# Performance work log

Measured on AMD Instinct MI355X. Metric: run time of the kernel, lower is better.

Reference implementation:

```python
import jax, jax.numpy as jnp
import numpy as np

B, C, HD, H, W = 4, 64, 64, 64, 64  # batch, input_dim, hidden_dim, spatial


def conv1x1(x, w, b):
    # x: [B, Cin, H, W], w: [Cout, Cin], b: [Cout]
    return jnp.einsum('oc,bchw->bohw', w, x) + b[None, :, None, None]


def setup_inputs() -> dict:
    key = jax.random.key(0)
    ks = jax.random.split(key, 16)
    sc = lambda cin: 1.0 / np.sqrt(cin)
    d = {
        'h': jax.random.normal(ks[0], (B, C, H, W), jnp.float32),
        'm': jax.random.normal(ks[1], (B, C, H, W), jnp.float32),
        'Wq': jax.random.normal(ks[2], (HD, C), jnp.float32) * sc(C),
        'bq': jnp.zeros((HD,), jnp.float32),
        'Wk': jax.random.normal(ks[3], (HD, C), jnp.float32) * sc(C),
        'bk': jnp.zeros((HD,), jnp.float32),
        'Wk2': jax.random.normal(ks[4], (HD, C), jnp.float32) * sc(C),
        'bk2': jnp.zeros((HD,), jnp.float32),
        'Wv': jax.random.normal(ks[5], (C, C), jnp.float32) * sc(C),
        'bv': jnp.zeros((C,), jnp.float32),
        'Wv2': jax.random.normal(ks[6], (C, C), jnp.float32) * sc(C),
        'bv2': jnp.zeros((C,), jnp.float32),
        'Wz': jax.random.normal(ks[7], (2 * C, 2 * C), jnp.float32) * sc(2 * C),
        'bz': jnp.zeros((2 * C,), jnp.float32),
        'Wm': jax.random.normal(ks[8], (3 * C, 3 * C), jnp.float32) * sc(3 * C),
        'bm': jnp.zeros((3 * C,), jnp.float32),
    }
    return d


def reference(h, m, Wq, bq, Wk, bk, Wk2, bk2, Wv, bv, Wv2, bv2, Wz, bz, Wm, bm):
    b, c, hh, ww = h.shape
    n = hh * ww
    K_h = conv1x1(h, Wk, bk).reshape(b, HD, n)            # [B, HD, N]
    Q_h = conv1x1(h, Wq, bq).reshape(b, HD, n).transpose(0, 2, 1)  # [B, N, HD]
    V_h = conv1x1(h, Wv, bv).reshape(b, c, n)             # [B, C, N]
    K_m = conv1x1(m, Wk2, bk2).reshape(b, HD, n)
    V_m = conv1x1(m, Wv2, bv2).reshape(b, c, n)

    A_h = jax.nn.softmax(jnp.einsum('bnd,bdk->bnk', Q_h, K_h), axis=-1)  # [B, N, N]
    Z_h = jnp.einsum('bnk,bck->bcn', A_h, V_h).reshape(b, c, hh, ww)
    A_m = jax.nn.softmax(jnp.einsum('bnd,bdk->bnk', Q_h, K_m), axis=-1)
    Z_m = jnp.einsum('bnk,bck->bcn', A_m, V_m).reshape(b, c, hh, ww)

    Z = conv1x1(jnp.concatenate([Z_h, Z_m], axis=1), Wz, bz)   # [B, 2C, H, W]
    combined = conv1x1(jnp.concatenate([Z, h], axis=1), Wm, bm)  # [B, 3C, H, W]
    mo, mg, mi = jnp.split(combined, 3, axis=1)
    mi = jax.nn.sigmoid(mi)
    new_m = (1.0 - mi) * m + mi * jnp.tanh(mg)
    new_h = jax.nn.sigmoid(mo) * new_m
    return (new_h, new_m)
```

## Files before the change

### kernel.cpp

```cpp
#include <hip/hip_runtime.h>

#define BN 4
#define NN 4096
#define SPLITK 4
#define KTILE 64
#define LOG2E 1.44269504f
#define MFIX 36.0f

typedef __attribute__((ext_vector_type(8))) __bf16 bf16x8;
typedef __attribute__((ext_vector_type(8))) short s16x8;
typedef __attribute__((ext_vector_type(4))) float f32x4;
typedef unsigned short u16;

__device__ __forceinline__ u16 f2bf(float x) {
  unsigned int u = __builtin_bit_cast(unsigned int, x);
  u = (u + 0x7fffu + ((u >> 16) & 1u)) >> 16;
  return (u16)u;
}
__device__ __forceinline__ u16 f2bfs(float x) {
  __bf16 b = (__bf16)x;
  return __builtin_bit_cast(u16, b);
}
__device__ __forceinline__ float bf2f(u16 s) {
  unsigned int u = ((unsigned int)s) << 16;
  return __builtin_bit_cast(float, u);
}

__device__ __forceinline__ float fexp2(float x) {
#if defined(__HIP_DEVICE_COMPILE__) && __has_builtin(__builtin_amdgcn_exp2f)
  return __builtin_amdgcn_exp2f(x);
#else
  return __builtin_exp2f(x);
#endif
}

__device__ __forceinline__ f32x4 mfma32(bf16x8 a, bf16x8 b, f32x4 c) {
#if defined(__HIP_DEVICE_COMPILE__)
  return __builtin_amdgcn_mfma_f32_16x16x32_bf16(a, b, c, 0, 0, 0);
#else
  (void)a; (void)b;
  return c;
#endif
}

__device__ __forceinline__ void gld16(const u16* g, u16* l) {
#if defined(__HIP_DEVICE_COMPILE__)
  __builtin_amdgcn_global_load_lds(
      (const __attribute__((address_space(1))) void*)g,
      (__attribute__((address_space(3))) void*)l, 16, 0, 0);
#else
  (void)g; (void)l;
#endif
}

#if defined(__HIP_DEVICE_COMPILE__)
#define SETPRIO(p) __builtin_amdgcn_s_setprio(p)
#else
#define SETPRIO(p)
#endif

__global__ __launch_bounds__(256) void fuse_w2_kernel(
    const float* __restrict__ Wz, const float* __restrict__ bz,
    const float* __restrict__ Wm, const float* __restrict__ bm,
    const float* __restrict__ Wq, const float* __restrict__ Wk,
    const float* __restrict__ Wk2, const float* __restrict__ Wv,
    const float* __restrict__ Wv2,
    u16* __restrict__ Wbig, float* __restrict__ bbig, u16* __restrict__ Wall) {
  __shared__ float wrow[128];
  __shared__ float bzs[128];
  int t = threadIdx.x;
  if (blockIdx.x >= 192) {
    int pid = blockIdx.x - 192;
    const float* Wsrc = pid == 0 ? Wq : pid == 1 ? Wk : pid == 2 ? Wk2 : pid == 3 ? Wv : Wv2;
    float sc = (pid == 0) ? LOG2E : 1.f;
#pragma unroll
    for (int i = 0; i < 16; ++i) {
      int idx = t * 16 + i;
      float w = Wsrc[idx] * sc;
      u16 hu = f2bf(w);
      Wall[pid * 4096 + idx] = hu;
      Wall[5 * 4096 + pid * 4096 + idx] = f2bf(w - bf2f(hu));
    }
    return;
  }
  int o = blockIdx.x;
  if (t < 128) { wrow[t] = Wm[o * 192 + t]; bzs[t] = bz[t]; }
  __syncthreads();
  if (t < 128) {
    float s = 0.f;
#pragma unroll 4
    for (int j = 0; j < 128; ++j) s = fmaf(wrow[j], Wz[j * 128 + t], s);
    Wbig[o * 192 + t] = f2bf(s);
  } else if (t < 192) {
    Wbig[o * 192 + t] = f2bf(Wm[o * 192 + t]);
  } else if (t == 192) {
    float s = bm[o];
    for (int j = 0; j < 128; ++j) s = fmaf(wrow[j], bzs[j], s);
    bbig[o] = s;
  }
}

__global__ __launch_bounds__(256) void proj7_kernel(
    const u16* __restrict__ Wall,
    const float* __restrict__ bq, const float* __restrict__ bk,
    const float* __restrict__ bk2, const float* __restrict__ bv,
    const float* __restrict__ bv2,
    const float* __restrict__ h, const float* __restrict__ m,
    u16* __restrict__ Q, u16* __restrict__ Kh, u16* __restrict__ Km,
    u16* __restrict__ Vh, u16* __restrict__ Vm, u16* __restrict__ hT) {
  __shared__ float xs[64][65];
  int blk = blockIdx.x;
  int nt = blk & 63, b = (blk >> 6) & 3, src_m = blk >> 8;
  const float* src = src_m ? m : h;
  int t = threadIdx.x, lane = t & 63, w = t >> 6, col = lane & 15, quad = lane >> 4;
  int n0 = nt * 64;
  {
    int c0 = w * 16, nl = lane;
#pragma unroll
    for (int i = 0; i < 16; ++i)
      xs[c0 + i][nl] = src[((size_t)(b * 64) + c0 + i) * NN + n0 + nl];
  }
  __syncthreads();
  int nloc = w * 16 + col;
  bf16x8 xh[2], xl[2];
#pragma unroll
  for (int half = 0; half < 2; ++half) {
    bf16x8 hh, ll;
#pragma unroll
    for (int j = 0; j < 8; ++j) {
      float x = xs[half * 32 + quad * 8 + j][nloc];
      u16 hu = f2bf(x);
      hh[j] = __builtin_bit_cast(__bf16, hu);
      ll[j] = (__bf16)(x - bf2f(hu));
    }
    xh[half] = hh; xl[half] = ll;
  }
  if (!src_m) {
    int cj = lane & 7, nr = lane >> 3;
#pragma unroll
    for (int it = 0; it < 2; ++it) {
      int n = w * 16 + it * 8 + nr;
      bf16x8 hi8;
#pragma unroll
      for (int i = 0; i < 8; ++i)
        hi8[i] = __builtin_bit_cast(__bf16, f2bf(xs[cj * 8 + i][n]));
      *(bf16x8*)(void*)(hT + ((size_t)b * NN + n0 + n) * 64 + cj * 8) = hi8;
    }
  }
  int glob_n = n0 + nloc;
  auto do_proj = [&](int pid, const float* bias, u16* dstQK, u16* dstV) {
    const u16* Whi = Wall + pid * 4096;
    const u16* Wlo = Wall + 5 * 4096 + pid * 4096;
    float sc = (pid == 0) ? LOG2E : 1.f;
#pragma unroll
    for (int ot = 0; ot < 4; ++ot) {
      size_t wb = (size_t)(ot * 16 + col) * 64 + quad * 8;
      bf16x8 wh0 = *(const bf16x8*)(const void*)(Whi + wb);
      bf16x8 wh1 = *(const bf16x8*)(const void*)(Whi + wb + 32);
      bf16x8 wl0 = *(const bf16x8*)(const void*)(Wlo + wb);
      bf16x8 wl1 = *(const bf16x8*)(const void*)(Wlo + wb + 32);
      float4 b4 = *(const float4*)(bias + ot * 16 + quad * 4);
      f32x4 c = {b4.x * sc, b4.y * sc, b4.z * sc, b4.w * sc};
      c = mfma32(wh0, xh[0], c);
      c = mfma32(wh1, xh[1], c);
      c = mfma32(wh0, xl[0], c);
      c = mfma32(wh1, xl[1], c);
      c = mfma32(wl0, xh[0], c);
      c = mfma32(wl1, xh[1], c);
      if (dstQK) {
        uint2 p;
        p.x = (unsigned)f2bf(c[0]) | ((unsigned)f2bf(c[1]) << 16);
        p.y = (unsigned)f2bf(c[2]) | ((unsigned)f2bf(c[3]) << 16);
        *(uint2*)(void*)(dstQK + ((size_t)b * NN + glob_n) * 64 + ot * 16 + quad * 4) = p;
      } else {
        size_t base = ((size_t)b << 18) + (size_t)(glob_n >> 5) * 2048 + ot * 512 +
                      (size_t)((glob_n >> 3) & 3) * 128 + (glob_n & 7);
#pragma unroll
        for (int r = 0; r < 4; ++r) dstV[base + (quad * 4 + r) * 8] = f2bf(c[r]);
      }
    }
  };
  if (!src_m) {
    do_proj(0, bq, Q, nullptr);
    do_proj(1, bk, Kh, nullptr);
    do_proj(3, bv, nullptr, Vh);
  } else {
    do_proj(2, bk2, Km, nullptr);
    do_proj(4, bv2, nullptr, Vm);
  }
}

__global__ __launch_bounds__(256, 4) void flash14_kernel(
    const u16* __restrict__ Qg, const u16* __restrict__ Khg,
    const u16* __restrict__ Kmg, const u16* __restrict__ Vhg,
    const u16* __restrict__ Vmg, u16* __restrict__ Opart,
    float* __restrict__ Lpart) {
  __shared__ u16 Kl[2][4096];
  __shared__ u16 Vl[3][4096];
  int blk = blockIdx.x;
  int combo = blk & 31, qt = blk >> 5;
  int attn = combo & 1, b = (combo >> 1) & 3, split = combo >> 3;
  const u16* K = (attn ? Kmg : Khg) + (size_t)b * NN * 64;
  const u16* V = (attn ? Vmg : Vhg) + ((size_t)b << 18);
  int t = threadIdx.x, wave = t >> 6, lane = t & 63, col = lane & 15, quad = lane >> 4;
  int row0 = qt * 128 + wave * 32;

  bf16x8 bq[2][2];
#pragma unroll
  for (int g = 0; g < 2; ++g) {
    const u16* qp = Qg + (size_t)b * NN * 64 + (size_t)(row0 + g * 16 + col) * 64 + quad * 8;
    bq[g][0] = *(const bf16x8*)(const void*)qp;
    bq[g][1] = *(const bf16x8*)(const void*)(qp + 32);
  }

  f32x4 O[2][4];
#pragma unroll
  for (int g = 0; g < 2; ++g)
#pragma unroll
    for (int i = 0; i < 4; ++i) O[g][i] = f32x4{0.f, 0.f, 0.f, 0.f};
  f32x4 Lacc[2];
  Lacc[0] = f32x4{0.f, 0.f, 0.f, 0.f};
  Lacc[1] = f32x4{0.f, 0.f, 0.f, 0.f};
  bf16x8 pa[2][2];
#pragma unroll
  for (int grp = 0; grp < 2; ++grp)
#pragma unroll
    for (int g = 0; g < 2; ++g) pa[grp][g] = bf16x8{};
  const f32x4 minit = {-MFIX, -MFIX, -MFIX, -MFIX};
  s16x8 onesv;
#pragma unroll
  for (int i = 0; i < 8; ++i) onesv[i] = (short)0x3F80;
  bf16x8 ones8 = __builtin_bit_cast(bf16x8, onesv);
  int sp = split * 8 + b * 2 + attn;

  const int kbase = split * (NN / SPLITK);
  const int TILES = NN / SPLITK / KTILE;

#define STAGE(KB, VB, K0)                                                        \
  _Pragma("unroll") for (int jj = 0; jj < 2; ++jj) {                             \
    int p = jj * 256 + t;                                                        \
    int krow_ = p >> 3;                                                          \
    int kj_ = (p & 7) ^ (krow_ & 7);                                             \
    int s5_ = krow_ & 31;                                                        \
    int tr_ = (krow_ & 32) | ((s5_ & 12) << 1) | (((s5_ >> 4) & 1) << 2) | (s5_ & 3); \
    gld16(K + (size_t)((K0) + tr_) * 64 + kj_ * 8, (KB) + p * 8);                \
    gld16(V + (size_t)(K0) * 64 + p * 8, (VB) + p * 8);                          \
  }

  STAGE(&Kl[0][0], &Vl[0][0], kbase);
  int vs_cur = 0;

  for (int kt = 0; kt < TILES; ++kt) {
    int cur = kt & 1;
    int vs_nxt = (vs_cur == 2) ? 0 : vs_cur + 1;
    int vs_prv = (vs_cur == 0) ? 2 : vs_cur - 1;
    __syncthreads();
    if (kt + 1 < TILES) {
      STAGE(&Kl[cur ^ 1][0], &Vl[vs_nxt][0], kbase + (kt + 1) * KTILE);
    }
    if (kt > 0) {
      const u16* vbase = &Vl[vs_prv][0] + lane * 8;
      SETPRIO(1);
#pragma unroll
      for (int grp = 0; grp < 2; ++grp)
#pragma unroll
        for (int ct = 0; ct < 4; ++ct) {
          bf16x8 vf = *(const bf16x8*)(const void*)(vbase + grp * 2048 + ct * 512);
          O[0][ct] = mfma32(pa[grp][0], vf, O[0][ct]);
          O[1][ct] = mfma32(pa[grp][1], vf, O[1][ct]);
        }
      SETPRIO(0);
    }
    const u16* Kb = &Kl[cur][0];
    f32x4 St[4][2];
    SETPRIO(1);
#pragma unroll
    for (int nt = 0; nt < 4; ++nt) {
      int row = nt * 16 + col;
      int ph0 = row * 8 + (quad ^ (col & 7));
      int ph1 = row * 8 + ((4 + quad) ^ (col & 7));
      bf16x8 a0 = *(const bf16x8*)(const void*)(Kb + ph0 * 8);
      bf16x8 a1 = *(const bf16x8*)(const void*)(Kb + ph1 * 8);
#pragma unroll
      for (int g = 0; g < 2; ++g) {
        f32x4 acc = mfma32(a0, bq[g][0], minit);
        acc = mfma32(a1, bq[g][1], acc);
        St[nt][g] = acc;
      }
    }
    SETPRIO(0);
#pragma unroll
    for (int grp = 0; grp < 2; ++grp)
#pragma unroll
      for (int g = 0; g < 2; ++g) {
        s16x8 pf;
#pragma unroll
        for (int r = 0; r < 4; ++r) {
          pf[r] = (short)f2bfs(fexp2(St[2 * grp][g][r]));
          pf[r + 4] = (short)f2bfs(fexp2(St[2 * grp + 1][g][r]));
        }
        bf16x8 p8 = __builtin_bit_cast(bf16x8, pf);
        pa[grp][g] = p8;
        Lacc[g] = mfma32(p8, ones8, Lacc[g]);
      }
    vs_cur = vs_nxt;
  }
#undef STAGE
  {
    int vs_prv = (vs_cur == 0) ? 2 : vs_cur - 1;
    const u16* vbase = &Vl[vs_prv][0] + lane * 8;
#pragma unroll
    for (int grp = 0; grp < 2; ++grp)
#pragma unroll
      for (int ct = 0; ct < 4; ++ct) {
        bf16x8 vf = *(const bf16x8*)(const void*)(vbase + grp * 2048 + ct * 512);
        O[0][ct] = mfma32(pa[grp][0], vf, O[0][ct]);
        O[1][ct] = mfma32(pa[grp][1], vf, O[1][ct]);
      }
  }

#pragma unroll
  for (int g = 0; g < 2; ++g) {
#pragma unroll
    for (int ct = 0; ct < 4; ++ct)
#pragma unroll
      for (int r = 0; r < 4; ++r) {
        size_t q = (size_t)row0 + g * 16 + quad * 4 + r;
        Opart[((size_t)sp * NN + q) * 64 + ct * 16 + col] = f2bfs(O[g][ct][r]);
      }
    if (col == 0) {
#pragma unroll
      for (int r = 0; r < 4; ++r)
        Lpart[(size_t)sp * NN + row0 + g * 16 + quad * 4 + r] = Lacc[g][r];
    }
  }
}

__global__ __launch_bounds__(256) void epi3_kernel(
    const u16* __restrict__ Wb, const float* __restrict__ bb,
    const u16* __restrict__ Opart, const float* __restrict__ Lpart,
    const u16* __restrict__ hT, const float* __restrict__ mglob,
    float* __restrict__ out) {
  int blk = blockIdx.x;
  int ng = blk * 16;
  int b = ng >> 12;
  int t = threadIdx.x, wave = t >> 6, lane = t & 63, col = lane & 15, quad = lane >> 4;
  int qb = (ng & (NN - 1)) + col;
  float Lh = 0.f, Lm = 0.f;
#pragma unroll
  for (int s = 0; s < SPLITK; ++s) {
    Lh += Lpart[(size_t)(s * 8 + b * 2) * NN + qb];
    Lm += Lpart[(size_t)(s * 8 + b * 2 + 1) * NN + qb];
  }
  float invLh = 1.f / Lh;
  float invLm = 1.f / Lm;
  size_t nrow = ((size_t)ng + col) * 64;
  bf16x8 bfr[6];
#define MERGEF(DST, ATTN, OFF, INVL)                                             \
  {                                                                              \
    float s8_[8] = {0.f, 0.f, 0.f, 0.f, 0.f, 0.f, 0.f, 0.f};                     \
    _Pragma("unroll") for (int sp_ = 0; sp_ < SPLITK; ++sp_) {                   \
      const u16* p_ =                                                            \
          Opart + ((size_t)(sp_ * 8 + b * 2 + (ATTN)) * NN + qb) * 64 + (OFF);   \
      bf16x8 a_ = *(const bf16x8*)(const void*)p_;                               \
      _Pragma("unroll") for (int i = 0; i < 8; ++i) s8_[i] += (float)a_[i];      \
    }                                                                            \
    bf16x8 r_;                                                                   \
    _Pragma("unroll") for (int i = 0; i < 8; ++i)                                \
      r_[i] = (__bf16)(s8_[i] * (INVL));                                         \
    DST = r_;                                                                    \
  }
  MERGEF(bfr[0], 0, quad * 8, invLh);
  MERGEF(bfr[1], 0, 32 + quad * 8, invLh);
  MERGEF(bfr[2], 1, quad * 8, invLm);
  MERGEF(bfr[3], 1, 32 + quad * 8, invLm);
#undef MERGEF
  bfr[4] = *(const bf16x8*)(const void*)(hT + nrow + quad * 8);
  bfr[5] = *(const bf16x8*)(const void*)(hT + nrow + 32 + quad * 8);
  f32x4 acc[3];
#pragma unroll
  for (int j = 0; j < 3; ++j) {
    int mt = wave + j * 4;
#pragma unroll
    for (int r = 0; r < 4; ++r) acc[j][r] = bb[mt * 16 + quad * 4 + r];
  }
#pragma unroll
  for (int ks = 0; ks < 6; ++ks) {
#pragma unroll
    for (int j = 0; j < 3; ++j) {
      int mt = wave + j * 4;
      bf16x8 af = *(const bf16x8*)(const void*)(Wb + (size_t)(mt * 16 + col) * 192 + ks * 32 + quad * 8);
      acc[j] = mfma32(af, bfr[ks], acc[j]);
    }
  }
  int nloc = (ng & (NN - 1)) + col;
#pragma unroll
  for (int r = 0; r < 4; ++r) {
    int o = wave * 16 + quad * 4 + r;
    float mo = acc[0][r], mgt = acc[1][r], mi = acc[2][r];
    float si = 1.f / (1.f + fexp2(-mi * LOG2E));
    float tg = 1.f - 2.f / (fexp2(2.f * LOG2E * mgt) + 1.f);
    float mv = mglob[(size_t)(b * 64 + o) * NN + nloc];
    float nm = (1.f - si) * mv + si * tg;
    float nh = nm / (1.f + fexp2(-mo * LOG2E));
    out[(size_t)(b * 64 + o) * NN + nloc] = nh;
    out[(size_t)BN * 64 * NN + (size_t)(b * 64 + o) * NN + nloc] = nm;
  }
}

extern "C" void kernel_launch(void* const* d_in, const int* in_sizes, int n_in,
                              void* d_out, int out_size, void* d_ws, size_t ws_size,
                              hipStream_t stream) {
  const float* h = (const float*)d_in[0];
  const float* m = (const float*)d_in[1];
  const float* Wq = (const float*)d_in[2];
  const float* bq = (const float*)d_in[3];
  const float* Wk = (const float*)d_in[4];
  const float* bk = (const float*)d_in[5];
  const float* Wk2 = (const float*)d_in[6];
  const float* bk2 = (const float*)d_in[7];
  const float* Wv = (const float*)d_in[8];
  const float* bv = (const float*)d_in[9];
  const float* Wv2 = (const float*)d_in[10];
  const float* bv2 = (const float*)d_in[11];
  const float* Wz = (const float*)d_in[12];
  const float* bz = (const float*)d_in[13];
  const float* Wm = (const float*)d_in[14];
  const float* bm = (const float*)d_in[15];
  float* out = (float*)d_out;

  size_t off = 0;
  auto alloc = [&](size_t bytes) {
    void* p = (char*)d_ws + off;
    off += (bytes + 255) & ~(size_t)255;
    return p;
  };
  const size_t bn64 = (size_t)BN * NN * 64;
  u16* Q  = (u16*)alloc(bn64 * 2);
  u16* Kh = (u16*)alloc(bn64 * 2);
  u16* Km = (u16*)alloc(bn64 * 2);
  u16* Vh = (u16*)alloc(bn64 * 2);
  u16* Vm = (u16*)alloc(bn64 * 2);
  u16* hT = (u16*)alloc(bn64 * 2);
  u16* Opart = (u16*)alloc((size_t)SPLITK * 8 * NN * 64 * 2);
  float* Lpart = (float*)alloc((size_t)SPLITK * 8 * NN * 4);
  u16* Wbigbf = (u16*)alloc(192 * 192 * 2);
  float* bbig = (float*)alloc(192 * 4);
  u16* Wall = (u16*)alloc((size_t)2 * 5 * 4096 * 2);
  (void)ws_size; (void)in_sizes; (void)n_in; (void)out_size;

  fuse_w2_kernel<<<197, 256, 0, stream>>>(Wz, bz, Wm, bm, Wq, Wk, Wk2, Wv, Wv2,
                                          Wbigbf, bbig, Wall);
  proj7_kernel<<<2 * BN * 64, 256, 0, stream>>>(Wall, bq, bk, bk2, bv, bv2, h, m,
                                                Q, Kh, Km, Vh, Vm, hT);
  flash14_kernel<<<32 * 32, 256, 0, stream>>>(Q, Kh, Km, Vh, Vm, Opart, Lpart);
  epi3_kernel<<<(BN * NN) / 16, 256, 0, stream>>>(Wbigbf, bbig, Opart, Lpart, hT, m, out);
}
```

Measured before the change: 167.3 us.

## Switch flash attention to 32x32x16 MFMA with matching V layout

```diff
diff --git a/kernel.cpp b/kernel.cpp
--- a/kernel.cpp
+++ b/kernel.cpp
@@ -10,6 +10,7 @@
 typedef __attribute__((ext_vector_type(8))) __bf16 bf16x8;
 typedef __attribute__((ext_vector_type(8))) short s16x8;
 typedef __attribute__((ext_vector_type(4))) float f32x4;
+typedef __attribute__((ext_vector_type(16))) float f32x16;
 typedef unsigned short u16;
 
 __device__ __forceinline__ u16 f2bf(float x) {
@@ -37,6 +38,15 @@
 __device__ __forceinline__ f32x4 mfma32(bf16x8 a, bf16x8 b, f32x4 c) {
 #if defined(__HIP_DEVICE_COMPILE__)
   return __builtin_amdgcn_mfma_f32_16x16x32_bf16(a, b, c, 0, 0, 0);
+#else
+  (void)a; (void)b;
+  return c;
+#endif
+}
+
+__device__ __forceinline__ f32x16 mfma3232(bf16x8 a, bf16x8 b, f32x16 c) {
+#if defined(__HIP_DEVICE_COMPILE__)
+  return __builtin_amdgcn_mfma_f32_32x32x16_bf16(a, b, c, 0, 0, 0);
 #else
   (void)a; (void)b;
   return c;
@@ -173,10 +183,16 @@
         p.y = (unsigned)f2bf(c[2]) | ((unsigned)f2bf(c[3]) << 16);
         *(uint2*)(void*)(dstQK + ((size_t)b * NN + glob_n) * 64 + ot * 16 + quad * 4) = p;
       } else {
-        size_t base = ((size_t)b << 18) + (size_t)(glob_n >> 5) * 2048 + ot * 512 +
-                      (size_t)((glob_n >> 3) & 3) * 128 + (glob_n & 7);
-#pragma unroll
-        for (int r = 0; r < 4; ++r) dstV[base + (quad * 4 + r) * 8] = f2bf(c[r]);
+        int kt_ = glob_n & 63;
+        int t_ = ((kt_ >> 5) << 1) | ((kt_ >> 4) & 1);
+        int w_ = kt_ & 15;
+        int hi_ = (w_ >> 2) & 1;
+        int j_ = (w_ & 3) | ((w_ & 8) >> 1);
+        size_t base2 = ((size_t)b << 18) + (size_t)(glob_n >> 6) * 4096 +
+                       (size_t)t_ * 1024 + hi_ * 8 + j_;
+#pragma unroll
+        for (int r = 0; r < 4; ++r)
+          dstV[base2 + ot * 256 + quad * 64 + r * 16] = f2bf(c[r]);
       }
     }
   };
@@ -190,7 +206,7 @@
   }
 }
 
-__global__ __launch_bounds__(256, 4) void flash14_kernel(
+__global__ __launch_bounds__(256, 4) void flash17_kernel(
     const u16* __restrict__ Qg, const u16* __restrict__ Khg,
     const u16* __restrict__ Kmg, const u16* __restrict__ Vhg,
     const u16* __restrict__ Vmg, u16* __restrict__ Opart,
@@ -202,35 +218,27 @@
   int attn = combo & 1, b = (combo >> 1) & 3, split = combo >> 3;
   const u16* K = (attn ? Kmg : Khg) + (size_t)b * NN * 64;
   const u16* V = (attn ? Vmg : Vhg) + ((size_t)b << 18);
-  int t = threadIdx.x, wave = t >> 6, lane = t & 63, col = lane & 15, quad = lane >> 4;
+  int t = threadIdx.x, wave = t >> 6, lane = t & 63;
+  int lq = lane & 31, hi = lane >> 5, l7 = lane & 7;
   int row0 = qt * 128 + wave * 32;
 
-  bf16x8 bq[2][2];
-#pragma unroll
-  for (int g = 0; g < 2; ++g) {
-    const u16* qp = Qg + (size_t)b * NN * 64 + (size_t)(row0 + g * 16 + col) * 64 + quad * 8;
-    bq[g][0] = *(const bf16x8*)(const void*)qp;
-    bq[g][1] = *(const bf16x8*)(const void*)(qp + 32);
-  }
-
-  f32x4 O[2][4];
-#pragma unroll
-  for (int g = 0; g < 2; ++g)
-#pragma unroll
-    for (int i = 0; i < 4; ++i) O[g][i] = f32x4{0.f, 0.f, 0.f, 0.f};
-  f32x4 Lacc[2];
-  Lacc[0] = f32x4{0.f, 0.f, 0.f, 0.f};
-  Lacc[1] = f32x4{0.f, 0.f, 0.f, 0.f};
-  bf16x8 pa[2][2];
-#pragma unroll
-  for (int grp = 0; grp < 2; ++grp)
-#pragma unroll
-    for (int g = 0; g < 2; ++g) pa[grp][g] = bf16x8{};
-  const f32x4 minit = {-MFIX, -MFIX, -MFIX, -MFIX};
-  s16x8 onesv;
-#pragma unroll
-  for (int i = 0; i < 8; ++i) onesv[i] = (short)0x3F80;
-  bf16x8 ones8 = __builtin_bit_cast(bf16x8, onesv);
+  bf16x8 bq[4];
+  const u16* qp = Qg + ((size_t)b * NN + row0 + lq) * 64 + hi * 8;
+#pragma unroll
+  for (int s = 0; s < 4; ++s) bq[s] = *(const bf16x8*)(const void*)(qp + s * 16);
+
+  f32x16 O[2];
+#pragma unroll
+  for (int cg = 0; cg < 2; ++cg)
+#pragma unroll
+    for (int i = 0; i < 16; ++i) O[cg][i] = 0.f;
+  float ls0 = 0.f, ls1 = 0.f, ls2 = 0.f, ls3 = 0.f;
+  bf16x8 pa[4];
+#pragma unroll
+  for (int i = 0; i < 4; ++i) pa[i] = bf16x8{};
+  f32x16 minit16;
+#pragma unroll
+  for (int i = 0; i < 16; ++i) minit16[i] = -MFIX;
   int sp = split * 8 + b * 2 + attn;
 
   const int kbase = split * (NN / SPLITK);
@@ -241,9 +249,7 @@
     int p = jj * 256 + t;                                                        \
     int krow_ = p >> 3;                                                          \
     int kj_ = (p & 7) ^ (krow_ & 7);                                             \
-    int s5_ = krow_ & 31;                                                        \
-    int tr_ = (krow_ & 32) | ((s5_ & 12) << 1) | (((s5_ >> 4) & 1) << 2) | (s5_ & 3); \
-    gld16(K + (size_t)((K0) + tr_) * 64 + kj_ * 8, (KB) + p * 8);                \
+    gld16(K + (size_t)((K0) + krow_) * 64 + kj_ * 8, (KB) + p * 8);              \
     gld16(V + (size_t)(K0) * 64 + p * 8, (VB) + p * 8);                          \
   }
 
@@ -259,81 +265,76 @@
       STAGE(&Kl[cur ^ 1][0], &Vl[vs_nxt][0], kbase + (kt + 1) * KTILE);
     }
     if (kt > 0) {
-      const u16* vbase = &Vl[vs_prv][0] + lane * 8;
+      const u16* vb = &Vl[vs_prv][0] + lq * 16 + hi * 8;
       SETPRIO(1);
 #pragma unroll
-      for (int grp = 0; grp < 2; ++grp)
-#pragma unroll
-        for (int ct = 0; ct < 4; ++ct) {
-          bf16x8 vf = *(const bf16x8*)(const void*)(vbase + grp * 2048 + ct * 512);
-          O[0][ct] = mfma32(pa[grp][0], vf, O[0][ct]);
-          O[1][ct] = mfma32(pa[grp][1], vf, O[1][ct]);
+      for (int cg = 0; cg < 2; ++cg)
+#pragma unroll
+        for (int tt = 0; tt < 4; ++tt) {
+          bf16x8 vf = *(const bf16x8*)(const void*)(vb + tt * 1024 + cg * 512);
+          O[cg] = mfma3232(vf, pa[tt], O[cg]);
         }
       SETPRIO(0);
     }
     const u16* Kb = &Kl[cur][0];
-    f32x4 St[4][2];
+    f32x16 St[2];
     SETPRIO(1);
 #pragma unroll
-    for (int nt = 0; nt < 4; ++nt) {
-      int row = nt * 16 + col;
-      int ph0 = row * 8 + (quad ^ (col & 7));
-      int ph1 = row * 8 + ((4 + quad) ^ (col & 7));
-      bf16x8 a0 = *(const bf16x8*)(const void*)(Kb + ph0 * 8);
-      bf16x8 a1 = *(const bf16x8*)(const void*)(Kb + ph1 * 8);
-#pragma unroll
-      for (int g = 0; g < 2; ++g) {
-        f32x4 acc = mfma32(a0, bq[g][0], minit);
-        acc = mfma32(a1, bq[g][1], acc);
-        St[nt][g] = acc;
+    for (int kg = 0; kg < 2; ++kg) {
+      const u16* kb = Kb + (kg * 32 + lq) * 64;
+      f32x16 acc = minit16;
+#pragma unroll
+      for (int s = 0; s < 4; ++s) {
+        bf16x8 aK = *(const bf16x8*)(const void*)(kb + ((2 * s + hi) ^ l7) * 8);
+        acc = mfma3232(aK, bq[s], acc);
       }
+      St[kg] = acc;
     }
     SETPRIO(0);
 #pragma unroll
-    for (int grp = 0; grp < 2; ++grp)
-#pragma unroll
-      for (int g = 0; g < 2; ++g) {
+    for (int kg = 0; kg < 2; ++kg)
+#pragma unroll
+      for (int half = 0; half < 2; ++half) {
         s16x8 pf;
 #pragma unroll
-        for (int r = 0; r < 4; ++r) {
-          pf[r] = (short)f2bfs(fexp2(St[2 * grp][g][r]));
-          pf[r + 4] = (short)f2bfs(fexp2(St[2 * grp + 1][g][r]));
+        for (int j = 0; j < 8; ++j) {
+          float e = fexp2(St[kg][half * 8 + j]);
+          if ((j & 3) == 0) ls0 += e;
+          else if ((j & 3) == 1) ls1 += e;
+          else if ((j & 3) == 2) ls2 += e;
+          else ls3 += e;
+          pf[j] = (short)f2bfs(e);
         }
-        bf16x8 p8 = __builtin_bit_cast(bf16x8, pf);
-        pa[grp][g] = p8;
-        Lacc[g] = mfma32(p8, ones8, Lacc[g]);
+        pa[kg * 2 + half] = __builtin_bit_cast(bf16x8, pf);
       }
     vs_cur = vs_nxt;
   }
 #undef STAGE
   {
     int vs_prv = (vs_cur == 0) ? 2 : vs_cur - 1;
-    const u16* vbase = &Vl[vs_prv][0] + lane * 8;
-#pragma unroll
-    for (int grp = 0; grp < 2; ++grp)
-#pragma unroll
-      for (int ct = 0; ct < 4; ++ct) {
-        bf16x8 vf = *(const bf16x8*)(const void*)(vbase + grp * 2048 + ct * 512);
-        O[0][ct] = mfma32(pa[grp][0], vf, O[0][ct]);
-        O[1][ct] = mfma32(pa[grp][1], vf, O[1][ct]);
+    const u16* vb = &Vl[vs_prv][0] + lq * 16 + hi * 8;
+#pragma unroll
+    for (int cg = 0; cg < 2; ++cg)
+#pragma unroll
+      for (int tt = 0; tt < 4; ++tt) {
+        bf16x8 vf = *(const bf16x8*)(const void*)(vb + tt * 1024 + cg * 512);
+        O[cg] = mfma3232(vf, pa[tt], O[cg]);
       }
   }
 
-#pragma unroll
-  for (int g = 0; g < 2; ++g) {
-#pragma unroll
-    for (int ct = 0; ct < 4; ++ct)
-#pragma unroll
-      for (int r = 0; r < 4; ++r) {
-        size_t q = (size_t)row0 + g * 16 + quad * 4 + r;
-        Opart[((size_t)sp * NN + q) * 64 + ct * 16 + col] = f2bfs(O[g][ct][r]);
-      }
-    if (col == 0) {
-#pragma unroll
-      for (int r = 0; r < 4; ++r)
-        Lpart[(size_t)sp * NN + row0 + g * 16 + quad * 4 + r] = Lacc[g][r];
-    }
-  }
+  size_t orow = ((size_t)sp * NN + row0 + lq) * 64;
+#pragma unroll
+  for (int cg = 0; cg < 2; ++cg)
+#pragma unroll
+    for (int rq = 0; rq < 4; ++rq) {
+      uint2 pk;
+      pk.x = (unsigned)f2bfs(O[cg][rq * 4]) | ((unsigned)f2bfs(O[cg][rq * 4 + 1]) << 16);
+      pk.y = (unsigned)f2bfs(O[cg][rq * 4 + 2]) | ((unsigned)f2bfs(O[cg][rq * 4 + 3]) << 16);
+      *(uint2*)(void*)(Opart + orow + cg * 32 + rq * 8 + hi * 4) = pk;
+    }
+  float lsum = (ls0 + ls1) + (ls2 + ls3);
+  float ltot = lsum + __shfl_xor(lsum, 32);
+  if (hi == 0) Lpart[(size_t)sp * NN + row0 + lq] = ltot;
 }
 
 __global__ __launch_bounds__(256) void epi3_kernel(
@@ -453,6 +454,6 @@
                                           Wbigbf, bbig, Wall);
   proj7_kernel<<<2 * BN * 64, 256, 0, stream>>>(Wall, bq, bk, bk2, bv, bv2, h, m,
                                                 Q, Kh, Km, Vh, Vm, hT);
-  flash14_kernel<<<32 * 32, 256, 0, stream>>>(Q, Kh, Km, Vh, Vm, Opart, Lpart);
+  flash17_kernel<<<32 * 32, 256, 0, stream>>>(Q, Kh, Km, Vh, Vm, Opart, Lpart);
   epi3_kernel<<<(BN * NN) / 16, 256, 0, stream>>>(Wbigbf, bbig, Opart, Lpart, hT, m, out);
 }
```

New measurement: 169.6 us. Within noise of the previous version (+1.4%).
